# Performance work log

Measured on AMD Instinct MI355X. Metric: run time of the kernel, lower is better.

## Reference

```python
import jax, jax.numpy as jnp
import numpy as np

N = 4096
IN_DIM = 512
OUT_DIM = 64
NUM_HEADS = 8
DENSITY = 0.01  # adjacency density


def setup_inputs() -> dict:
    key = jax.random.key(0)
    ks = jax.random.split(key, 9)
    h = jax.random.normal(ks[0], (N, IN_DIM), dtype=jnp.float32)
    # sparse adjacency realized as a dense 0/1 mask (the module calls A.to_dense())
    A = (jax.random.uniform(ks[1], (N, N)) < DENSITY).astype(jnp.float32)
    s_in = 1.0 / np.sqrt(IN_DIM)
    Wq = jax.random.normal(ks[2], (IN_DIM, OUT_DIM * NUM_HEADS), dtype=jnp.float32) * s_in
    bq = jax.random.normal(ks[3], (OUT_DIM * NUM_HEADS,), dtype=jnp.float32) * s_in
    Wk = jax.random.normal(ks[4], (IN_DIM, OUT_DIM * NUM_HEADS), dtype=jnp.float32) * s_in
    bk = jax.random.normal(ks[5], (OUT_DIM * NUM_HEADS,), dtype=jnp.float32) * s_in
    Wv = jax.random.normal(ks[6], (IN_DIM, OUT_DIM * NUM_HEADS), dtype=jnp.float32) * s_in
    bv = jax.random.normal(ks[7], (OUT_DIM * NUM_HEADS,), dtype=jnp.float32) * s_in
    return {"A": A, "h": h, "Wq": Wq, "bq": bq, "Wk": Wk, "bk": bk, "Wv": Wv, "bv": bv}


def reference(A, h, Wq, bq, Wk, bk, Wv, bv):
    n = h.shape[0]
    scaling = OUT_DIM ** (-0.5)
    # (N, out_dim, H) to match torch .reshape(N, out_dim, num_heads)
    q = ((h @ Wq) + bq).reshape(n, OUT_DIM, NUM_HEADS) * scaling
    k = ((h @ Wk) + bk).reshape(n, OUT_DIM, NUM_HEADS)
    v = ((h @ Wv) + bv).reshape(n, OUT_DIM, NUM_HEADS)
    # attn[h,n,m] = sum_d q[n,d,h] * k[m,d,h], masked by dense adjacency
    attn = jnp.einsum('ndh,mdh->hnm', q, k) * A[None, :, :]
    # NOTE: original code softmaxes over dim=0 == the HEAD axis (faithful)
    attn = jax.nn.softmax(attn, axis=0)
    # out[h,n,d] = sum_m attn[h,n,m] * v[m,d,h]
    out = jnp.einsum('hnm,mdh->hnd', attn, v)
    # raw row-major reshape of (H, N, D) -> (N, H*D), as in the original
    return out.reshape(n, -1)
```

## Files before the change

### kernel.cpp

```cpp
#include <hip/hip_runtime.h>

typedef unsigned short u16;
typedef unsigned short u16x8 __attribute__((ext_vector_type(8)));
typedef __bf16 bf16x8 __attribute__((ext_vector_type(8)));
typedef float f32x4 __attribute__((ext_vector_type(4)));

#define NN 4096
#define KD 512
#define HD 512
#define CAP 112

__device__ __forceinline__ u16 f2bf(float f) {
    unsigned u = __builtin_bit_cast(unsigned, f);
    u += 0x7fffu + ((u >> 16) & 1u);
    return (u16)(u >> 16);
}
__device__ __forceinline__ float bf2f(u16 u) {
    return __builtin_bit_cast(float, ((unsigned)u) << 16);
}
__device__ __forceinline__ int permj(int j) { return ((j & 7) << 6) | (j >> 3); }

#define GLOAD16(gp, lp) \
    __builtin_amdgcn_global_load_lds((const __attribute__((address_space(1))) void*)(gp), \
                                     (__attribute__((address_space(3))) void*)(lp), 16, 0, 0)

__global__ void k_cvt_h(const float4* __restrict__ in, u16* __restrict__ out) {
    int i = blockIdx.x * blockDim.x + threadIdx.x;
    float4 f = in[i];
    ((ushort4*)out)[i] = make_ushort4(f2bf(f.x), f2bf(f.y), f2bf(f.z), f2bf(f.w));
}

__global__ void k_w(const float* __restrict__ Wq, const float* __restrict__ Wk,
                    const float* __restrict__ Wv, const float* __restrict__ bq,
                    const float* __restrict__ bk, const float* __restrict__ bvp,
                    u16* __restrict__ wt, float* __restrict__ pbias) {
    __shared__ float tile[32][33];
    int z = blockIdx.z;
    const float* W = (z == 0) ? Wq : ((z == 1) ? Wk : Wv);
    float scale = (z == 0) ? 0.125f : 1.0f;
    int j0 = blockIdx.x * 32, k0 = blockIdx.y * 32;
    int tx = threadIdx.x, ty = threadIdx.y;
    #pragma unroll
    for (int r = 0; r < 32; r += 8)
        tile[ty + r][tx] = W[(size_t)(k0 + ty + r) * HD + j0 + tx];
    __syncthreads();
    #pragma unroll
    for (int r = 0; r < 32; r += 8) {
        int j = j0 + ty + r;
        wt[(size_t)(z * 512 + permj(j)) * KD + k0 + tx] = f2bf(scale * tile[tx][ty + r]);
    }
    if (blockIdx.y == 0 && ty == 0) {
        int j = j0 + tx;
        float b = (z == 0) ? bq[j] * 0.125f : ((z == 1) ? bk[j] : bvp[j]);
        pbias[z * 512 + permj(j)] = b;
    }
}

__global__ __launch_bounds__(256) void k_gemm(const u16* __restrict__ hb,
        const u16* __restrict__ wt, const float* __restrict__ pbias,
        float* __restrict__ qbuf, u16* __restrict__ kbuf, u16* __restrict__ vbuf)
{
    __shared__ u16 As[128 * 64];
    __shared__ u16 Bs[128 * 64];
    const int tid = threadIdx.x;
    const int w = tid >> 6, lane = tid & 63;
    const int wr = w >> 1, wc = w & 1;
    const int l16 = lane & 15, half = lane >> 4;
    const int row0 = blockIdx.x * 128, col0 = blockIdx.y * 128;
    const int la = lane & 7, lb = lane >> 3;
    const int swcol = ((la ^ lb) << 3);

    const u16* gA[4]; const u16* gB[4];
    u16* lA[4]; u16* lB[4];
    #pragma unroll
    for (int s = 0; s < 4; ++s) {
        int i = w * 4 + s;
        gA[s] = hb + (size_t)(row0 + 8 * i + lb) * KD + swcol;
        gB[s] = wt + (size_t)(col0 + 8 * i + lb) * KD + swcol;
        lA[s] = As + i * 512;
        lB[s] = Bs + i * 512;
    }

    f32x4 acc[4][4] = {};

    for (int kk = 0; kk < KD; kk += 64) {
        #pragma unroll
        for (int s = 0; s < 4; ++s) {
            GLOAD16(gA[s] + kk, lA[s]);
            GLOAD16(gB[s] + kk, lB[s]);
        }
        __syncthreads();
        #pragma unroll
        for (int kk2 = 0; kk2 < 2; ++kk2) {
            bf16x8 af[4], bf[4];
            #pragma unroll
            for (int mi = 0; mi < 4; ++mi) {
                int row = wr * 64 + mi * 16 + l16;
                int off = row * 128 + (((kk2 << 6) | (half << 4)) ^ ((l16 & 7) << 4));
                af[mi] = *(const bf16x8*)((const char*)As + off);
            }
            #pragma unroll
            for (int ni = 0; ni < 4; ++ni) {
                int row = wc * 64 + ni * 16 + l16;
                int off = row * 128 + (((kk2 << 6) | (half << 4)) ^ ((l16 & 7) << 4));
                bf[ni] = *(const bf16x8*)((const char*)Bs + off);
            }
            #pragma unroll
            for (int mi = 0; mi < 4; ++mi)
                #pragma unroll
                for (int ni = 0; ni < 4; ++ni)
                    acc[mi][ni] = __builtin_amdgcn_mfma_f32_16x16x32_bf16(
                        af[mi], bf[ni], acc[mi][ni], 0, 0, 0);
        }
        __syncthreads();
    }

    const int seg = blockIdx.y >> 2;
    #pragma unroll
    for (int ni = 0; ni < 4; ++ni) {
        int j = col0 + wc * 64 + ni * 16 + l16;
        float bj = pbias[j];
        #pragma unroll
        for (int mi = 0; mi < 4; ++mi) {
            #pragma unroll
            for (int r = 0; r < 4; ++r) {
                int m = row0 + wr * 64 + mi * 16 + half * 4 + r;
                float val = acc[mi][ni][r] + bj;
                if (seg == 0)      qbuf[(size_t)m * 512 + j] = val;
                else if (seg == 1) kbuf[(size_t)m * 512 + (j - 512)] = f2bf(val);
                else               vbuf[(size_t)m * 512 + (j - 1024)] = f2bf(val);
            }
        }
    }
}

__global__ __launch_bounds__(256) void k_colsum(const u16* __restrict__ vbuf,
                                                float* __restrict__ colsum) {
    const int tid = threadIdx.x, w = tid >> 6, lane = tid & 63;
    __shared__ float s_col[512];
    s_col[tid] = 0.f; s_col[tid + 256] = 0.f;
    __syncthreads();
    const int row0 = (blockIdx.x * 4 + w) * 16;
    float acc8[8] = {0.f,0.f,0.f,0.f,0.f,0.f,0.f,0.f};
    #pragma unroll
    for (int rr = 0; rr < 16; ++rr) {
        u16x8 v8 = *(const u16x8*)(vbuf + (size_t)(row0 + rr) * 512 + lane * 8);
        #pragma unroll
        for (int j = 0; j < 8; ++j) acc8[j] += bf2f(v8[j]);
    }
    #pragma unroll
    for (int j = 0; j < 8; ++j) atomicAdd(&s_col[lane * 8 + j], acc8[j]);
    __syncthreads();
    atomicAdd(&colsum[tid], s_col[tid]);
    atomicAdd(&colsum[tid + 256], s_col[tid + 256]);
}

__global__ __launch_bounds__(256) void k_attn(const float4* __restrict__ A4,
        const float* __restrict__ qbuf, const u16* __restrict__ kbuf,
        const u16* __restrict__ vbuf, const float* __restrict__ colsum,
        float* __restrict__ out)
{
    const int tid = threadIdx.x, w = tid >> 6, lane = tid & 63;
    const int n0 = blockIdx.x * 8;
    __shared__ int   s_cnt[8];
    __shared__ u16   s_idx[8][CAP];
    __shared__ float s_q[8][512];
    __shared__ float s_c[8][CAP][8];

    if (tid < 8) s_cnt[tid] = 0;
    __syncthreads();

    {
        const float4* qg = (const float4*)(qbuf + (size_t)n0 * 512);
        float4* qs = (float4*)&s_q[0][0];
        #pragma unroll
        for (int jj = 0; jj < 4; ++jj) qs[jj * 256 + tid] = qg[jj * 256 + tid];
    }
    {
        const float4* arow = A4 + (size_t)n0 * 1024;
        #pragma unroll
        for (int ii = 0; ii < 32; ++ii) {
            int i = ii * 256 + tid;
            float4 a = arow[i];
            if (a.x != 0.f || a.y != 0.f || a.z != 0.f || a.w != 0.f) {
                int r = i >> 10, m0 = (i & 1023) * 4;
                if (a.x != 0.f) { int p = atomicAdd(&s_cnt[r], 1); if (p < CAP) s_idx[r][p] = (u16)m0; }
                if (a.y != 0.f) { int p = atomicAdd(&s_cnt[r], 1); if (p < CAP) s_idx[r][p] = (u16)(m0 + 1); }
                if (a.z != 0.f) { int p = atomicAdd(&s_cnt[r], 1); if (p < CAP) s_idx[r][p] = (u16)(m0 + 2); }
                if (a.w != 0.f) { int p = atomicAdd(&s_cnt[r], 1); if (p < CAP) s_idx[r][p] = (u16)(m0 + 3); }
            }
        }
    }
    __syncthreads();

    for (int rr = 0; rr < 2; ++rr) {
        const int r = 2 * w + rr;
        const int cnt = min(s_cnt[r], CAP);
        for (int base = 0; base < cnt; base += 64) {
            const int e = base + lane;
            if (e < cnt) {
                const int m = s_idx[r][e];
                const u16* kr = kbuf + (size_t)m * 512;
                float acc8[8] = {0.f,0.f,0.f,0.f,0.f,0.f,0.f,0.f};
                #pragma unroll 8
                for (int c = 0; c < 64; ++c) {
                    u16x8 kv = *(const u16x8*)(kr + c * 8);
                    const float* qp = &s_q[r][c * 8];
                    float p = qp[0]*bf2f(kv[0]) + qp[1]*bf2f(kv[1]) + qp[2]*bf2f(kv[2]) + qp[3]*bf2f(kv[3])
                            + qp[4]*bf2f(kv[4]) + qp[5]*bf2f(kv[5]) + qp[6]*bf2f(kv[6]) + qp[7]*bf2f(kv[7]);
                    acc8[c >> 3] += p;
                }
                float mx = acc8[0];
                #pragma unroll
                for (int i = 1; i < 8; ++i) mx = fmaxf(mx, acc8[i]);
                float Z = 0.f;
                #pragma unroll
                for (int i = 0; i < 8; ++i) { acc8[i] = __expf(acc8[i] - mx); Z += acc8[i]; }
                const float rz = 1.f / Z;
                #pragma unroll
                for (int i = 0; i < 8; ++i) s_c[r][e][i] = acc8[i] * rz - 0.125f;
            }
        }
    }

    const int hh = lane >> 3, dbase = (lane & 7) * 8;
    const float4 cs0 = *(const float4*)(colsum + lane * 8);
    const float4 cs1 = *(const float4*)(colsum + lane * 8 + 4);
    for (int rr = 0; rr < 2; ++rr) {
        const int r = 2 * w + rr;
        const int cnt = min(s_cnt[r], CAP);
        float acc8[8] = {0.f,0.f,0.f,0.f,0.f,0.f,0.f,0.f};
        int e = 0;
        for (; e + 4 <= cnt; e += 4) {
            int m0 = s_idx[r][e], m1 = s_idx[r][e+1], m2 = s_idx[r][e+2], m3 = s_idx[r][e+3];
            float c0 = s_c[r][e][hh],   c1 = s_c[r][e+1][hh];
            float c2 = s_c[r][e+2][hh], c3 = s_c[r][e+3][hh];
            u16x8 v0 = *(const u16x8*)(vbuf + (size_t)m0 * 512 + lane * 8);
            u16x8 v1 = *(const u16x8*)(vbuf + (size_t)m1 * 512 + lane * 8);
            u16x8 v2 = *(const u16x8*)(vbuf + (size_t)m2 * 512 + lane * 8);
            u16x8 v3 = *(const u16x8*)(vbuf + (size_t)m3 * 512 + lane * 8);
            #pragma unroll
            for (int j = 0; j < 8; ++j)
                acc8[j] += c0*bf2f(v0[j]) + c1*bf2f(v1[j]) + c2*bf2f(v2[j]) + c3*bf2f(v3[j]);
        }
        for (; e < cnt; ++e) {
            int m = s_idx[r][e];
            float c = s_c[r][e][hh];
            u16x8 vv = *(const u16x8*)(vbuf + (size_t)m * 512 + lane * 8);
            #pragma unroll
            for (int j = 0; j < 8; ++j) acc8[j] += c * bf2f(vv[j]);
        }
        f32x4 o0, o1;
        o0[0] = acc8[0] + 0.125f * cs0.x; o0[1] = acc8[1] + 0.125f * cs0.y;
        o0[2] = acc8[2] + 0.125f * cs0.z; o0[3] = acc8[3] + 0.125f * cs0.w;
        o1[0] = acc8[4] + 0.125f * cs1.x; o1[1] = acc8[5] + 0.125f * cs1.y;
        o1[2] = acc8[6] + 0.125f * cs1.z; o1[3] = acc8[7] + 0.125f * cs1.w;
        float* op = out + (size_t)hh * (NN * 64) + (size_t)(n0 + r) * 64 + dbase;
        *(f32x4*)op = o0;
        *(f32x4*)(op + 4) = o1;
    }
}

extern "C" void kernel_launch(void* const* d_in, const int* in_sizes, int n_in,
                              void* d_out, int out_size, void* d_ws, size_t ws_size,
                              hipStream_t stream)
{
    const float* A  = (const float*)d_in[0];
    const float* h  = (const float*)d_in[1];
    const float* Wq = (const float*)d_in[2];
    const float* bq = (const float*)d_in[3];
    const float* Wk = (const float*)d_in[4];
    const float* bk = (const float*)d_in[5];
    const float* Wv = (const float*)d_in[6];
    const float* bv = (const float*)d_in[7];
    float* out = (float*)d_out;

    char* ws = (char*)d_ws;
    float* qbuf   = (float*)(ws);
    u16*   kbuf   = (u16*)(ws + (8u  << 20));
    u16*   vbuf   = (u16*)(ws + (12u << 20));
    u16*   hb     = (u16*)(ws + (16u << 20));
    u16*   wt     = (u16*)(ws + (20u << 20));
    float* pbias  = (float*)(ws + (22u << 20));
    float* colsum = (float*)(ws + (22u << 20) + 8192);

    k_cvt_h<<<dim3(2048), dim3(256), 0, stream>>>((const float4*)h, hb);
    k_w<<<dim3(16, 16, 3), dim3(32, 8), 0, stream>>>(Wq, Wk, Wv, bq, bk, bv, wt, pbias);
    hipMemsetAsync(colsum, 0, 512 * sizeof(float), stream);
    k_gemm<<<dim3(32, 12), dim3(256), 0, stream>>>(hb, wt, pbias, qbuf, kbuf, vbuf);
    k_colsum<<<dim3(64), dim3(256), 0, stream>>>(vbuf, colsum);
    k_attn<<<dim3(512), dim3(256), 0, stream>>>((const float4*)A, qbuf, kbuf, vbuf, colsum, out);
}
```

Baseline: 191.5 us.

## Fuse prep kernels, fold colsum into GEMM epilogue, repartition attention to 2 rows per block

Merges the h conversion and weight transpose into one prep launch. The column-sum kernel is removed: V column sums are now accumulated with shuffles and atomics inside the GEMM epilogue. Q is stored as bf16 instead of fp32, and the attention coefficients in shared memory are also held as bf16. The attention kernel now handles 2 rows per block (2048 blocks) with the edge list split across two wave pairs and reduced through shared memory, and CAP drops to 96. This cuts launch count and memory traffic and improves occupancy, at the cost of lower precision for q and the coefficients, and a tighter cap on neighbors per row.

Result: slower. 204.4 us (+6.8%).

```diff
diff --git a/kernel.cpp b/kernel.cpp
--- a/kernel.cpp
+++ b/kernel.cpp
@@ -8,7 +8,7 @@
 #define NN 4096
 #define KD 512
 #define HD 512
-#define CAP 112
+#define CAP 96
 
 __device__ __forceinline__ u16 f2bf(float f) {
     unsigned u = __builtin_bit_cast(unsigned, f);
@@ -24,22 +24,27 @@
     __builtin_amdgcn_global_load_lds((const __attribute__((address_space(1))) void*)(gp), \
                                      (__attribute__((address_space(3))) void*)(lp), 16, 0, 0)
 
-__global__ void k_cvt_h(const float4* __restrict__ in, u16* __restrict__ out) {
-    int i = blockIdx.x * blockDim.x + threadIdx.x;
-    float4 f = in[i];
-    ((ushort4*)out)[i] = make_ushort4(f2bf(f.x), f2bf(f.y), f2bf(f.z), f2bf(f.w));
-}
-
-__global__ void k_w(const float* __restrict__ Wq, const float* __restrict__ Wk,
-                    const float* __restrict__ Wv, const float* __restrict__ bq,
-                    const float* __restrict__ bk, const float* __restrict__ bvp,
-                    u16* __restrict__ wt, float* __restrict__ pbias) {
+__global__ __launch_bounds__(256) void k_prep(const float4* __restrict__ h4,
+        u16* __restrict__ hb,
+        const float* __restrict__ Wq, const float* __restrict__ Wk,
+        const float* __restrict__ Wv, const float* __restrict__ bq,
+        const float* __restrict__ bk, const float* __restrict__ bv,
+        u16* __restrict__ wt, float* __restrict__ pbias)
+{
     __shared__ float tile[32][33];
-    int z = blockIdx.z;
+    const int tid = threadIdx.x;
+    if (blockIdx.x < 2048) {
+        int i = blockIdx.x * 256 + tid;
+        float4 f = h4[i];
+        ((ushort4*)hb)[i] = make_ushort4(f2bf(f.x), f2bf(f.y), f2bf(f.z), f2bf(f.w));
+        return;
+    }
+    const int b2 = blockIdx.x - 2048;
+    const int jb = b2 & 15, kb = (b2 >> 4) & 15, z = b2 >> 8;
     const float* W = (z == 0) ? Wq : ((z == 1) ? Wk : Wv);
-    float scale = (z == 0) ? 0.125f : 1.0f;
-    int j0 = blockIdx.x * 32, k0 = blockIdx.y * 32;
-    int tx = threadIdx.x, ty = threadIdx.y;
+    const float scale = (z == 0) ? 0.125f : 1.0f;
+    const int j0 = jb * 32, k0 = kb * 32;
+    const int tx = tid & 31, ty = tid >> 5;
     #pragma unroll
     for (int r = 0; r < 32; r += 8)
         tile[ty + r][tx] = W[(size_t)(k0 + ty + r) * HD + j0 + tx];
@@ -49,16 +54,17 @@
         int j = j0 + ty + r;
         wt[(size_t)(z * 512 + permj(j)) * KD + k0 + tx] = f2bf(scale * tile[tx][ty + r]);
     }
-    if (blockIdx.y == 0 && ty == 0) {
+    if (kb == 0 && ty == 0) {
         int j = j0 + tx;
-        float b = (z == 0) ? bq[j] * 0.125f : ((z == 1) ? bk[j] : bvp[j]);
+        float b = (z == 0) ? bq[j] * 0.125f : ((z == 1) ? bk[j] : bv[j]);
         pbias[z * 512 + permj(j)] = b;
     }
 }
 
 __global__ __launch_bounds__(256) void k_gemm(const u16* __restrict__ hb,
         const u16* __restrict__ wt, const float* __restrict__ pbias,
-        float* __restrict__ qbuf, u16* __restrict__ kbuf, u16* __restrict__ vbuf)
+        u16* __restrict__ qbuf, u16* __restrict__ kbuf, u16* __restrict__ vbuf,
+        float* __restrict__ colsum)
 {
     __shared__ u16 As[128 * 64];
     __shared__ u16 Bs[128 * 64];
@@ -120,66 +126,48 @@
     for (int ni = 0; ni < 4; ++ni) {
         int j = col0 + wc * 64 + ni * 16 + l16;
         float bj = pbias[j];
+        float csum = 0.f;
         #pragma unroll
         for (int mi = 0; mi < 4; ++mi) {
             #pragma unroll
             for (int r = 0; r < 4; ++r) {
                 int m = row0 + wr * 64 + mi * 16 + half * 4 + r;
                 float val = acc[mi][ni][r] + bj;
-                if (seg == 0)      qbuf[(size_t)m * 512 + j] = val;
+                if (seg == 0)      qbuf[(size_t)m * 512 + j] = f2bf(val);
                 else if (seg == 1) kbuf[(size_t)m * 512 + (j - 512)] = f2bf(val);
-                else               vbuf[(size_t)m * 512 + (j - 1024)] = f2bf(val);
-            }
-        }
-    }
-}
-
-__global__ __launch_bounds__(256) void k_colsum(const u16* __restrict__ vbuf,
-                                                float* __restrict__ colsum) {
-    const int tid = threadIdx.x, w = tid >> 6, lane = tid & 63;
-    __shared__ float s_col[512];
-    s_col[tid] = 0.f; s_col[tid + 256] = 0.f;
-    __syncthreads();
-    const int row0 = (blockIdx.x * 4 + w) * 16;
-    float acc8[8] = {0.f,0.f,0.f,0.f,0.f,0.f,0.f,0.f};
-    #pragma unroll
-    for (int rr = 0; rr < 16; ++rr) {
-        u16x8 v8 = *(const u16x8*)(vbuf + (size_t)(row0 + rr) * 512 + lane * 8);
-        #pragma unroll
-        for (int j = 0; j < 8; ++j) acc8[j] += bf2f(v8[j]);
-    }
-    #pragma unroll
-    for (int j = 0; j < 8; ++j) atomicAdd(&s_col[lane * 8 + j], acc8[j]);
-    __syncthreads();
-    atomicAdd(&colsum[tid], s_col[tid]);
-    atomicAdd(&colsum[tid + 256], s_col[tid + 256]);
+                else             { vbuf[(size_t)m * 512 + (j - 1024)] = f2bf(val); csum += val; }
+            }
+        }
+        if (seg == 2) {
+            csum += __shfl_xor(csum, 16);
+            csum += __shfl_xor(csum, 32);
+            if (lane < 16) atomicAdd(&colsum[j - 1024], csum);
+        }
+    }
 }
 
 __global__ __launch_bounds__(256) void k_attn(const float4* __restrict__ A4,
-        const float* __restrict__ qbuf, const u16* __restrict__ kbuf,
+        const u16* __restrict__ qbuf, const u16* __restrict__ kbuf,
         const u16* __restrict__ vbuf, const float* __restrict__ colsum,
         float* __restrict__ out)
 {
     const int tid = threadIdx.x, w = tid >> 6, lane = tid & 63;
-    const int n0 = blockIdx.x * 8;
-    __shared__ int   s_cnt[8];
-    __shared__ u16   s_idx[8][CAP];
-    __shared__ float s_q[8][512];
-    __shared__ float s_c[8][CAP][8];
-
-    if (tid < 8) s_cnt[tid] = 0;
-    __syncthreads();
-
-    {
-        const float4* qg = (const float4*)(qbuf + (size_t)n0 * 512);
-        float4* qs = (float4*)&s_q[0][0];
-        #pragma unroll
-        for (int jj = 0; jj < 4; ++jj) qs[jj * 256 + tid] = qg[jj * 256 + tid];
-    }
+    const int n0 = blockIdx.x * 2;
+    const int row = w & 1, seg = w >> 1;
+    __shared__ u16   s_q[2][512];
+    __shared__ u16   s_idx[2][CAP];
+    __shared__ u16   s_c[2][CAP][8];
+    __shared__ float s_red[2][2][512];
+    __shared__ int   s_cnt[2];
+
+    if (tid < 2) s_cnt[tid] = 0;
+    ((ushort4*)&s_q[0][0])[tid] = ((const ushort4*)(qbuf + (size_t)n0 * 512))[tid];
+    __syncthreads();
+
     {
         const float4* arow = A4 + (size_t)n0 * 1024;
         #pragma unroll
-        for (int ii = 0; ii < 32; ++ii) {
+        for (int ii = 0; ii < 8; ++ii) {
             int i = ii * 256 + tid;
             float4 a = arow[i];
             if (a.x != 0.f || a.y != 0.f || a.z != 0.f || a.w != 0.f) {
@@ -192,49 +180,47 @@
         }
     }
     __syncthreads();
-
-    for (int rr = 0; rr < 2; ++rr) {
-        const int r = 2 * w + rr;
-        const int cnt = min(s_cnt[r], CAP);
-        for (int base = 0; base < cnt; base += 64) {
-            const int e = base + lane;
-            if (e < cnt) {
-                const int m = s_idx[r][e];
-                const u16* kr = kbuf + (size_t)m * 512;
-                float acc8[8] = {0.f,0.f,0.f,0.f,0.f,0.f,0.f,0.f};
-                #pragma unroll 8
-                for (int c = 0; c < 64; ++c) {
-                    u16x8 kv = *(const u16x8*)(kr + c * 8);
-                    const float* qp = &s_q[r][c * 8];
-                    float p = qp[0]*bf2f(kv[0]) + qp[1]*bf2f(kv[1]) + qp[2]*bf2f(kv[2]) + qp[3]*bf2f(kv[3])
-                            + qp[4]*bf2f(kv[4]) + qp[5]*bf2f(kv[5]) + qp[6]*bf2f(kv[6]) + qp[7]*bf2f(kv[7]);
-                    acc8[c >> 3] += p;
-                }
-                float mx = acc8[0];
-                #pragma unroll
-                for (int i = 1; i < 8; ++i) mx = fmaxf(mx, acc8[i]);
-                float Z = 0.f;
-                #pragma unroll
-                for (int i = 0; i < 8; ++i) { acc8[i] = __expf(acc8[i] - mx); Z += acc8[i]; }
-                const float rz = 1.f / Z;
-                #pragma unroll
-                for (int i = 0; i < 8; ++i) s_c[r][e][i] = acc8[i] * rz - 0.125f;
-            }
-        }
-    }
-
-    const int hh = lane >> 3, dbase = (lane & 7) * 8;
-    const float4 cs0 = *(const float4*)(colsum + lane * 8);
-    const float4 cs1 = *(const float4*)(colsum + lane * 8 + 4);
-    for (int rr = 0; rr < 2; ++rr) {
-        const int r = 2 * w + rr;
-        const int cnt = min(s_cnt[r], CAP);
-        float acc8[8] = {0.f,0.f,0.f,0.f,0.f,0.f,0.f,0.f};
-        int e = 0;
-        for (; e + 4 <= cnt; e += 4) {
-            int m0 = s_idx[r][e], m1 = s_idx[r][e+1], m2 = s_idx[r][e+2], m3 = s_idx[r][e+3];
-            float c0 = s_c[r][e][hh],   c1 = s_c[r][e+1][hh];
-            float c2 = s_c[r][e+2][hh], c3 = s_c[r][e+3][hh];
+    const int cnt = min(s_cnt[row], CAP);
+
+    {
+        const int e = 2 * lane + seg;
+        if (e < cnt) {
+            const int m = s_idx[row][e];
+            const u16* kr = kbuf + (size_t)m * 512;
+            float acc8[8] = {0.f,0.f,0.f,0.f,0.f,0.f,0.f,0.f};
+            #pragma unroll 8
+            for (int c = 0; c < 64; ++c) {
+                u16x8 kv = *(const u16x8*)(kr + c * 8);
+                u16x8 qv = *(const u16x8*)&s_q[row][c * 8];
+                float p = bf2f(qv[0])*bf2f(kv[0]) + bf2f(qv[1])*bf2f(kv[1])
+                        + bf2f(qv[2])*bf2f(kv[2]) + bf2f(qv[3])*bf2f(kv[3])
+                        + bf2f(qv[4])*bf2f(kv[4]) + bf2f(qv[5])*bf2f(kv[5])
+                        + bf2f(qv[6])*bf2f(kv[6]) + bf2f(qv[7])*bf2f(kv[7]);
+                acc8[c >> 3] += p;
+            }
+            float mx = acc8[0];
+            #pragma unroll
+            for (int i = 1; i < 8; ++i) mx = fmaxf(mx, acc8[i]);
+            float Z = 0.f;
+            #pragma unroll
+            for (int i = 0; i < 8; ++i) { acc8[i] = __expf(acc8[i] - mx); Z += acc8[i]; }
+            const float rz = 1.f / Z;
+            u16x8 st;
+            #pragma unroll
+            for (int i = 0; i < 8; ++i) st[i] = f2bf(acc8[i] * rz - 0.125f);
+            *(u16x8*)&s_c[row][e][0] = st;
+        }
+    }
+
+    const int hh = lane >> 3;
+    float acc8[8] = {0.f,0.f,0.f,0.f,0.f,0.f,0.f,0.f};
+    {
+        int e = seg;
+        for (; e + 6 < cnt; e += 8) {
+            int m0 = s_idx[row][e],     m1 = s_idx[row][e + 2];
+            int m2 = s_idx[row][e + 4], m3 = s_idx[row][e + 6];
+            float c0 = bf2f(s_c[row][e][hh]),     c1 = bf2f(s_c[row][e + 2][hh]);
+            float c2 = bf2f(s_c[row][e + 4][hh]), c3 = bf2f(s_c[row][e + 6][hh]);
             u16x8 v0 = *(const u16x8*)(vbuf + (size_t)m0 * 512 + lane * 8);
             u16x8 v1 = *(const u16x8*)(vbuf + (size_t)m1 * 512 + lane * 8);
             u16x8 v2 = *(const u16x8*)(vbuf + (size_t)m2 * 512 + lane * 8);
@@ -243,21 +229,30 @@
             for (int j = 0; j < 8; ++j)
                 acc8[j] += c0*bf2f(v0[j]) + c1*bf2f(v1[j]) + c2*bf2f(v2[j]) + c3*bf2f(v3[j]);
         }
-        for (; e < cnt; ++e) {
-            int m = s_idx[r][e];
-            float c = s_c[r][e][hh];
+        for (; e < cnt; e += 2) {
+            int m = s_idx[row][e];
+            float c = bf2f(s_c[row][e][hh]);
             u16x8 vv = *(const u16x8*)(vbuf + (size_t)m * 512 + lane * 8);
             #pragma unroll
             for (int j = 0; j < 8; ++j) acc8[j] += c * bf2f(vv[j]);
         }
-        f32x4 o0, o1;
-        o0[0] = acc8[0] + 0.125f * cs0.x; o0[1] = acc8[1] + 0.125f * cs0.y;
-        o0[2] = acc8[2] + 0.125f * cs0.z; o0[3] = acc8[3] + 0.125f * cs0.w;
-        o1[0] = acc8[4] + 0.125f * cs1.x; o1[1] = acc8[5] + 0.125f * cs1.y;
-        o1[2] = acc8[6] + 0.125f * cs1.z; o1[3] = acc8[7] + 0.125f * cs1.w;
-        float* op = out + (size_t)hh * (NN * 64) + (size_t)(n0 + r) * 64 + dbase;
-        *(f32x4*)op = o0;
-        *(f32x4*)(op + 4) = o1;
+    }
+    {
+        f32x4 r0, r1;
+        r0[0]=acc8[0]; r0[1]=acc8[1]; r0[2]=acc8[2]; r0[3]=acc8[3];
+        r1[0]=acc8[4]; r1[1]=acc8[5]; r1[2]=acc8[6]; r1[3]=acc8[7];
+        *(f32x4*)&s_red[seg][row][lane * 8]     = r0;
+        *(f32x4*)&s_red[seg][row][lane * 8 + 4] = r1;
+    }
+    __syncthreads();
+
+    #pragma unroll
+    for (int p = 0; p < 4; ++p) {
+        int idx = p * 256 + tid;
+        int rr = idx >> 9, i2 = idx & 511;
+        int hh2 = i2 >> 6, d = i2 & 63;
+        float val = s_red[0][rr][i2] + s_red[1][rr][i2] + 0.125f * colsum[i2];
+        out[(size_t)hh2 * (NN * 64) + (size_t)(n0 + rr) * 64 + d] = val;
     }
 }
 
@@ -276,18 +271,17 @@
     float* out = (float*)d_out;
 
     char* ws = (char*)d_ws;
-    float* qbuf   = (float*)(ws);
-    u16*   kbuf   = (u16*)(ws + (8u  << 20));
-    u16*   vbuf   = (u16*)(ws + (12u << 20));
-    u16*   hb     = (u16*)(ws + (16u << 20));
-    u16*   wt     = (u16*)(ws + (20u << 20));
-    float* pbias  = (float*)(ws + (22u << 20));
-    float* colsum = (float*)(ws + (22u << 20) + 8192);
-
-    k_cvt_h<<<dim3(2048), dim3(256), 0, stream>>>((const float4*)h, hb);
-    k_w<<<dim3(16, 16, 3), dim3(32, 8), 0, stream>>>(Wq, Wk, Wv, bq, bk, bv, wt, pbias);
+    u16*   qbuf   = (u16*)(ws);
+    u16*   kbuf   = (u16*)(ws + (4u  << 20));
+    u16*   vbuf   = (u16*)(ws + (8u  << 20));
+    u16*   hb     = (u16*)(ws + (12u << 20));
+    u16*   wt     = (u16*)(ws + (16u << 20));
+    float* pbias  = (float*)(ws + (18u << 20));
+    float* colsum = (float*)(ws + (18u << 20) + 8192);
+
     hipMemsetAsync(colsum, 0, 512 * sizeof(float), stream);
-    k_gemm<<<dim3(32, 12), dim3(256), 0, stream>>>(hb, wt, pbias, qbuf, kbuf, vbuf);
-    k_colsum<<<dim3(64), dim3(256), 0, stream>>>(vbuf, colsum);
-    k_attn<<<dim3(512), dim3(256), 0, stream>>>((const float4*)A, qbuf, kbuf, vbuf, colsum, out);
-}
+    k_prep<<<dim3(2816), dim3(256), 0, stream>>>((const float4*)h, hb,
+            Wq, Wk, Wv, bq, bk, bv, wt, pbias);
+    k_gemm<<<dim3(32, 12), dim3(256), 0, stream>>>(hb, wt, pbias, qbuf, kbuf, vbuf, colsum);
+    k_attn<<<dim3(2048), dim3(256), 0, stream>>>((const float4*)A, qbuf, kbuf, vbuf, colsum, out);
+}
```
